# Performance work log

Hardware: AMD Instinct MI355X
Metric: run time of the kernel (lower is better)

## Reference

```python
import jax, jax.numpy as jnp
import numpy as np

B, CI, H, W = 16, 32, 224, 224
CO, K, STRIDE = 32, 3, 1


def setup_inputs() -> dict:
    key = jax.random.key(0)
    k1, k2, k3 = jax.random.split(key, 3)
    x = jax.random.normal(k1, (B, CI, H, W), dtype=jnp.float32)
    weights = jax.random.normal(k2, (CO, CI, K, K), dtype=jnp.float32)
    bias = jax.random.normal(k3, (CO,), dtype=jnp.float32)
    return {"x": x, "weights": weights, "bias": bias}


def reference(x, weights, bias):
    # Faithful to HandmadeConv2D with padding=0, stride=1: a VALID
    # cross-correlation (the torch code never actually pads x) plus bias.
    out = jax.lax.conv_general_dilated(
        x, weights,
        window_strides=(STRIDE, STRIDE),
        padding="VALID",
        dimension_numbers=("NCHW", "OIHW", "NCHW"),
    )
    return out + bias[None, :, None, None]
```

## Files before the change

### kernel.cpp

```cpp
#include <hip/hip_runtime.h>
#include <hip/hip_bf16.h>

#define B_  16
#define CI_ 32
#define H_  224
#define W_  224
#define CO_ 32
#define OH_ 222
#define OW_ 222
#define HW_ (H_*W_)
#define K_  288

#define OHB   8
#define ROWS  10
#define OWT   64
#define PXT   66
#define NOHB  28
#define NOWT  4
#define NTASK (ROWS*PXT)
#define NBLK  (NOHB*NOWT*B_)

typedef __attribute__((ext_vector_type(8))) short short8;
typedef __attribute__((ext_vector_type(4))) float float4v;
typedef float float4u __attribute__((ext_vector_type(4), aligned(4)));

__global__ void wprep(const float* __restrict__ w, unsigned short* __restrict__ wbf) {
    int idx = blockIdx.x * 256 + threadIdx.x;
    if (idx >= CO_ * K_) return;
    int co  = idx / K_;
    int rem = idx - co * K_;
    int ci  = rem / 9;
    int g   = rem - ci * 9;
    unsigned int u = __float_as_uint(w[idx]);
    u = u + 0x7FFFu + ((u >> 16) & 1u);
    wbf[co * K_ + g * 32 + ci] = (unsigned short)(u >> 16);
}

__global__ __launch_bounds__(512, 4) void conv_fused(
    const float* __restrict__ x, const unsigned short* __restrict__ wbf,
    const float* __restrict__ bias, float* __restrict__ out)
{
    __shared__ unsigned short Xs[NTASK * CI_];

    const int t   = threadIdx.x;
    const int bid = blockIdx.x;
    const int xcd   = bid & 7;
    const int owt   = (bid >> 3) & 3;
    const int gid   = (bid >> 5) * 8 + xcd;
    const int b     = gid / NOHB;
    const int ohblk = gid - b * NOHB;
    const int r0    = ohblk * OHB;
    const int ow0   = owt * OWT;

    for (int task = t; task < NTASK; task += 512) {
        const int tr = task / PXT;
        const int p  = task - tr * PXT;
        int row = r0 + tr;  if (row > H_ - 1) row = H_ - 1;
        int col = ow0 + p;  if (col > W_ - 1) col = W_ - 1;
        const float* xp = x + (size_t)b * CI_ * HW_ + (size_t)row * W_ + col;
        unsigned short* dst = &Xs[task * CI_];
#pragma unroll
        for (int h = 0; h < 2; ++h) {
            float f[16];
#pragma unroll
            for (int j = 0; j < 16; ++j) f[j] = xp[(size_t)(h * 16 + j) * HW_];
            union { short8 s8[2]; __hip_bfloat162 h2[8]; } u;
#pragma unroll
            for (int i = 0; i < 8; ++i)
                u.h2[i] = __float22bfloat162_rn(make_float2(f[2*i], f[2*i+1]));
            *(short8*)&dst[h * 16]     = u.s8[0];
            *(short8*)&dst[h * 16 + 8] = u.s8[1];
        }
    }
    __syncthreads();

    const int lane = t & 63;
    const int wv   = t >> 6;
    const int oh   = r0 + wv;
    if (oh >= OH_) return;
    const int i16  = lane & 15;
    const int quad = lane >> 4;

    const unsigned short* wr0 = wbf + (size_t)i16 * K_;
    const unsigned short* wr1 = wbf + (size_t)(16 + i16) * K_;

    float4v acc[4][2] = {};

#pragma unroll
    for (int g = 0; g < 9; ++g) {
        const int kh = g / 3;
        const int kw = g - kh * 3;
        const short8 b0 = *(const short8*)&wr0[g * 32 + quad * 8];
        const short8 b1 = *(const short8*)&wr1[g * 32 + quad * 8];
        const unsigned short* ar =
            &Xs[((wv + kh) * PXT + i16 + kw) * CI_ + quad * 8];
#pragma unroll
        for (int ot = 0; ot < 4; ++ot) {
            const short8 a = *(const short8*)&ar[ot * 16 * CI_];
            acc[ot][0] = __builtin_amdgcn_mfma_f32_16x16x32_bf16(a, b0, acc[ot][0], 0, 0, 0);
            acc[ot][1] = __builtin_amdgcn_mfma_f32_16x16x32_bf16(a, b1, acc[ot][1], 0, 0, 0);
        }
    }

    const float bv0 = bias[i16];
    const float bv1 = bias[16 + i16];
    const size_t o0 = ((size_t)(b * CO_ + i16) * OH_ + oh) * (size_t)OW_;
    const size_t o1 = ((size_t)(b * CO_ + 16 + i16) * OH_ + oh) * (size_t)OW_;
#pragma unroll
    for (int ot = 0; ot < 4; ++ot) {
        const int owq = ow0 + ot * 16 + quad * 4;
        float4u v0 = { acc[ot][0][0] + bv0, acc[ot][0][1] + bv0,
                       acc[ot][0][2] + bv0, acc[ot][0][3] + bv0 };
        float4u v1 = { acc[ot][1][0] + bv1, acc[ot][1][1] + bv1,
                       acc[ot][1][2] + bv1, acc[ot][1][3] + bv1 };
        if (owq + 3 < OW_) {
            *(float4u*)&out[o0 + owq] = v0;
            *(float4u*)&out[o1 + owq] = v1;
        } else {
#pragma unroll
            for (int r = 0; r < 4; ++r) {
                if (owq + r < OW_) {
                    out[o0 + owq + r] = acc[ot][0][r] + bv0;
                    out[o1 + owq + r] = acc[ot][1][r] + bv1;
                }
            }
        }
    }
}

extern "C" void kernel_launch(void* const* d_in, const int* in_sizes, int n_in,
                              void* d_out, int out_size, void* d_ws, size_t ws_size,
                              hipStream_t stream) {
    const float* x    = (const float*)d_in[0];
    const float* w    = (const float*)d_in[1];
    const float* bias = (const float*)d_in[2];
    float* out        = (float*)d_out;
    unsigned short* wbf = (unsigned short*)d_ws;

    wprep<<<(CO_ * K_ + 255) / 256, 256, 0, stream>>>(w, wbf);
    conv_fused<<<dim3(NBLK), 512, 0, stream>>>(x, wbf, bias, out);
}
```

Before: 224.8 us.

## Load input column pairs with float2 and XOR-swizzle LDS layout to avoid bank conflicts

Each thread now loads two adjacent columns per channel with float2 global loads, so one pass covers the tile instead of a strided task loop. The shared-memory tile is XOR-swizzled on 16-byte chunks so the MFMA A-operand reads and the staging writes avoid LDS bank conflicts. The occupancy hint in launch_bounds is raised from 4 to 6 blocks. In exchange there is more address arithmetic, the last odd column is duplicated at the edge, and the higher occupancy target may force register limits.

```diff
diff --git a/kernel.cpp b/kernel.cpp
--- a/kernel.cpp
+++ b/kernel.cpp
@@ -17,12 +17,16 @@
 #define PXT   66
 #define NOHB  28
 #define NOWT  4
-#define NTASK (ROWS*PXT)
+#define NPAIR (ROWS*(PXT/2))
 #define NBLK  (NOHB*NOWT*B_)
 
 typedef __attribute__((ext_vector_type(8))) short short8;
 typedef __attribute__((ext_vector_type(4))) float float4v;
 typedef float float4u __attribute__((ext_vector_type(4), aligned(4)));
+
+__device__ __forceinline__ unsigned swz(unsigned L) {
+    return L ^ (((L >> 7) & 7u) << 4);
+}
 
 __global__ void wprep(const float* __restrict__ w, unsigned short* __restrict__ wbf) {
     int idx = blockIdx.x * 256 + threadIdx.x;
@@ -36,11 +40,11 @@
     wbf[co * K_ + g * 32 + ci] = (unsigned short)(u >> 16);
 }
 
-__global__ __launch_bounds__(512, 4) void conv_fused(
+__global__ __launch_bounds__(512, 6) void conv_fused(
     const float* __restrict__ x, const unsigned short* __restrict__ wbf,
     const float* __restrict__ bias, float* __restrict__ out)
 {
-    __shared__ unsigned short Xs[NTASK * CI_];
+    __shared__ unsigned short Xs[ROWS * PXT * CI_];
 
     const int t   = threadIdx.x;
     const int bid = blockIdx.x;
@@ -52,24 +56,38 @@
     const int r0    = ohblk * OHB;
     const int ow0   = owt * OWT;
 
-    for (int task = t; task < NTASK; task += 512) {
-        const int tr = task / PXT;
-        const int p  = task - tr * PXT;
+    if (t < NPAIR) {
+        const int tr = t / (PXT / 2);
+        const int j  = t - tr * (PXT / 2);
         int row = r0 + tr;  if (row > H_ - 1) row = H_ - 1;
-        int col = ow0 + p;  if (col > W_ - 1) col = W_ - 1;
-        const float* xp = x + (size_t)b * CI_ * HW_ + (size_t)row * W_ + col;
-        unsigned short* dst = &Xs[task * CI_];
+        const int c = ow0 + 2 * j;
+        const float* xp = x + (size_t)b * CI_ * HW_ + (size_t)row * W_;
+        const unsigned base = (unsigned)(tr * PXT + 2 * j) * 64u;
 #pragma unroll
         for (int h = 0; h < 2; ++h) {
-            float f[16];
+            float2 f2[16];
+            if (c + 1 < W_) {
 #pragma unroll
-            for (int j = 0; j < 16; ++j) f[j] = xp[(size_t)(h * 16 + j) * HW_];
-            union { short8 s8[2]; __hip_bfloat162 h2[8]; } u;
+                for (int i = 0; i < 16; ++i)
+                    f2[i] = *(const float2*)&xp[(size_t)(h * 16 + i) * HW_ + c];
+            } else {
 #pragma unroll
-            for (int i = 0; i < 8; ++i)
-                u.h2[i] = __float22bfloat162_rn(make_float2(f[2*i], f[2*i+1]));
-            *(short8*)&dst[h * 16]     = u.s8[0];
-            *(short8*)&dst[h * 16 + 8] = u.s8[1];
+                for (int i = 0; i < 16; ++i) {
+                    float s = xp[(size_t)(h * 16 + i) * HW_ + (W_ - 1)];
+                    f2[i] = make_float2(s, s);
+                }
+            }
+            union { short8 s8[4]; __hip_bfloat162 h2[16]; } u;
+#pragma unroll
+            for (int i = 0; i < 8; ++i) {
+                u.h2[i]     = __float22bfloat162_rn(make_float2(f2[2*i].x, f2[2*i+1].x));
+                u.h2[8 + i] = __float22bfloat162_rn(make_float2(f2[2*i].y, f2[2*i+1].y));
+            }
+#pragma unroll
+            for (int q2 = 0; q2 < 4; ++q2) {
+                const int cc = (q2 < 2) ? (2 * h + q2) : (4 + 2 * h + (q2 - 2));
+                *(short8*)((char*)Xs + swz(base + (unsigned)cc * 16u)) = u.s8[q2];
+            }
         }
     }
     __syncthreads();
@@ -92,11 +110,11 @@
         const int kw = g - kh * 3;
         const short8 b0 = *(const short8*)&wr0[g * 32 + quad * 8];
         const short8 b1 = *(const short8*)&wr1[g * 32 + quad * 8];
-        const unsigned short* ar =
-            &Xs[((wv + kh) * PXT + i16 + kw) * CI_ + quad * 8];
+        const unsigned rowbase = (unsigned)((wv + kh) * PXT) * 64u + (unsigned)quad * 16u;
 #pragma unroll
         for (int ot = 0; ot < 4; ++ot) {
-            const short8 a = *(const short8*)&ar[ot * 16 * CI_];
+            const unsigned L = rowbase + (unsigned)(ot * 16 + i16 + kw) * 64u;
+            const short8 a = *(const short8*)((const char*)Xs + swz(L));
             acc[ot][0] = __builtin_amdgcn_mfma_f32_16x16x32_bf16(a, b0, acc[ot][0], 0, 0, 0);
             acc[ot][1] = __builtin_amdgcn_mfma_f32_16x16x32_bf16(a, b1, acc[ot][1], 0, 0, 0);
         }
```

Result: no change. 223.5 us (-0.6%).
